# Performance work log

Hardware: AMD Instinct MI355X
Metric: run time of the kernel (lower is better)

The kernel has to match this reference:

```python
import jax, jax.numpy as jnp
import numpy as np

N_NODES = 100000
N_EDGES = 6400000


def setup_inputs() -> dict:
    key = jax.random.key(0)
    k1, k2, k3, k4, k5, k6 = jax.random.split(key, 6)
    x = jax.random.normal(k1, (N_NODES, 10), dtype=jnp.float32)
    edge_index = jax.random.randint(k2, (2, N_EDGES), 0, N_NODES, dtype=jnp.int64)
    # GCNConv(10,16) and GCNConv(16,2) parameters (glorot-ish scale)
    W1 = jax.random.normal(k3, (10, 16), dtype=jnp.float32) * (1.0 / np.sqrt(10))
    b1 = jnp.zeros((16,), dtype=jnp.float32)
    W2 = jax.random.normal(k4, (16, 2), dtype=jnp.float32) * (1.0 / np.sqrt(16))
    b2 = jnp.zeros((2,), dtype=jnp.float32)
    return {"x": x, "edge_index": edge_index, "W1": W1, "b1": b1, "W2": W2, "b2": b2}


def _gcn_conv(h, src, dst, norm, W, b, n_nodes):
    # PyG GCNConv: linear first, then normalized scatter-add aggregation
    h = h @ W                                   # [N, out]
    msg = h[src] * norm[:, None]                # gather + per-edge scale
    out = jax.ops.segment_sum(msg, dst, num_segments=n_nodes)
    return out + b


def reference(x, edge_index, W1, b1, W2, b2):
    n_nodes = x.shape[0]
    loop = jnp.arange(n_nodes, dtype=edge_index.dtype)
    src = jnp.concatenate([edge_index[0], loop])  # self-loops added (PyG default)
    dst = jnp.concatenate([edge_index[1], loop])
    # symmetric normalization deg^{-1/2} A_hat deg^{-1/2} (deg from target index)
    deg = jax.ops.segment_sum(jnp.ones_like(dst, dtype=x.dtype), dst, num_segments=n_nodes)
    dinv = jnp.where(deg > 0, jax.lax.rsqrt(deg), 0.0)
    norm = dinv[src] * dinv[dst]                 # [E+N]
    h = _gcn_conv(x, src, dst, norm, W1, b1, n_nodes)
    h = jax.nn.relu(h)
    out = _gcn_conv(h, src, dst, norm, W2, b2, n_nodes)
    return out
```

## Files before the change

### kernel.cpp

```cpp
#include <hip/hip_runtime.h>
#include <hip/hip_fp16.h>


#define BKT_BITS  8
#define BKT_SZ    256
#define NBK       512
#define NBLKA     256
#define TPB_A     1024
#define TPB_B     512
#define DST_SHIFT 24
#define SRC_MASK  0xFFFFFFu
#define XS_BYTES  32

static __device__ __forceinline__ int nt_src(const void* ei, int is64, int n_edges, unsigned e) {
    return is64 ? (int)__builtin_nontemporal_load(&((const long long*)ei)[e])
                : __builtin_nontemporal_load(&((const int*)ei)[e]);
}
static __device__ __forceinline__ int nt_dst(const void* ei, int is64, int n_edges, unsigned e) {
    return is64 ? (int)__builtin_nontemporal_load(&((const long long*)ei)[(unsigned)n_edges + e])
                : __builtin_nontemporal_load(&((const int*)ei)[(unsigned)n_edges + e]);
}

static __device__ __forceinline__ float2 h2f(unsigned w) {
    __half2 h = *(__half2*)&w;
    return __half22float2(h);
}

static __global__ void detect64_kernel(const unsigned int* __restrict__ w, int* flag) {
    __shared__ int nz;
    if (threadIdx.x == 0) nz = 0;
    __syncthreads();
    int local = 0;
    for (int k = threadIdx.x; k < 4096; k += blockDim.x)
        if (w[2 * k + 1] != 0u) local = 1;
    if (local) atomicOr(&nz, 1);
    __syncthreads();
    if (threadIdx.x == 0) *flag = (nz == 0) ? 1 : 0;
}

static __global__ void histA_kernel(const void* __restrict__ ei, const int* __restrict__ flag,
                                    unsigned* __restrict__ histA, int n_edges) {
    __shared__ unsigned h[NBK];
    for (int i = threadIdx.x; i < NBK; i += TPB_A) h[i] = 0u;
    __syncthreads();
    const int is64 = *flag;
    unsigned stride = gridDim.x * blockDim.x;
    for (unsigned e = blockIdx.x * blockDim.x + threadIdx.x; e < (unsigned)n_edges; e += stride) {
        int d = nt_dst(ei, is64, n_edges, e);
        atomicAdd(&h[(unsigned)d >> BKT_BITS], 1u);
    }
    __syncthreads();
    for (int i = threadIdx.x; i < NBK; i += TPB_A)
        histA[blockIdx.x * NBK + i] = h[i];
}

static __global__ void scan1_kernel(unsigned* __restrict__ histA, unsigned* __restrict__ total) {
    __shared__ unsigned s0[NBLKA], s1[NBLKA];
    const int b = blockIdx.x;
    const int t = threadIdx.x;
    unsigned v = histA[t * NBK + b];
    unsigned* a = s0; unsigned* c = s1;
    a[t] = v;
    __syncthreads();
    for (int off = 1; off < NBLKA; off <<= 1) {
        c[t] = a[t] + (t >= off ? a[t - off] : 0u);
        __syncthreads();
        unsigned* tmp = a; a = c; c = tmp;
    }
    histA[t * NBK + b] = a[t] - v;
    if (t == NBLKA - 1) total[b] = a[NBLKA - 1];
}

static __global__ void scan2_kernel(const unsigned* __restrict__ total,
                                    unsigned* __restrict__ bucket_base) {
    __shared__ unsigned s0[NBK], s1[NBK];
    const int t = threadIdx.x;
    unsigned v = total[t];
    unsigned* a = s0; unsigned* c = s1;
    a[t] = v;
    __syncthreads();
    for (int off = 1; off < NBK; off <<= 1) {
        c[t] = a[t] + (t >= off ? a[t - off] : 0u);
        __syncthreads();
        unsigned* tmp = a; a = c; c = tmp;
    }
    bucket_base[t] = a[t] - v;
}

static __global__ void scatterA_kernel(const void* __restrict__ ei, const int* __restrict__ flag,
                                       const unsigned* __restrict__ histA,
                                       const unsigned* __restrict__ bucket_base,
                                       unsigned* __restrict__ bucketed, int n_edges) {
    __shared__ unsigned cur[NBK];
    for (int i = threadIdx.x; i < NBK; i += TPB_A)
        cur[i] = bucket_base[i] + histA[blockIdx.x * NBK + i];
    __syncthreads();
    const int is64 = *flag;
    unsigned stride = gridDim.x * blockDim.x;
    for (unsigned e = blockIdx.x * blockDim.x + threadIdx.x; e < (unsigned)n_edges; e += stride) {
        unsigned s = (unsigned)nt_src(ei, is64, n_edges, e);
        unsigned d = (unsigned)nt_dst(ei, is64, n_edges, e);
        unsigned pos = atomicAdd(&cur[d >> BKT_BITS], 1u);
        bucketed[pos] = s | ((d & (BKT_SZ - 1u)) << DST_SHIFT);
    }
}

static __global__ void passB_kernel(const unsigned* __restrict__ bucketed,
                                    const unsigned* __restrict__ total,
                                    const unsigned* __restrict__ bucket_base,
                                    const float* __restrict__ x,
                                    unsigned* __restrict__ csr_src,
                                    unsigned* __restrict__ row_start,
                                    unsigned* __restrict__ cnt,
                                    float* __restrict__ dinv,
                                    char* __restrict__ xs, int n_nodes) {
    const int b = blockIdx.x;
    const int n0 = b << BKT_BITS;
    const int t = threadIdx.x;
    const unsigned base = bucket_base[b];
    const unsigned count = total[b];

    __shared__ unsigned h[BKT_SZ];
    __shared__ unsigned s0[BKT_SZ], s1[BKT_SZ];
    __shared__ unsigned cur[BKT_SZ];
    if (t < BKT_SZ) h[t] = 0u;
    __syncthreads();
    for (unsigned k = t; k < count; k += TPB_B)
        atomicAdd(&h[bucketed[base + k] >> DST_SHIFT], 1u);
    __syncthreads();
    unsigned* a = s0; unsigned* c = s1;
    if (t < BKT_SZ) a[t] = h[t];
    __syncthreads();
    for (int off = 1; off < BKT_SZ; off <<= 1) {
        if (t < BKT_SZ) c[t] = a[t] + (t >= off ? a[t - off] : 0u);
        __syncthreads();
        unsigned* tmp = a; a = c; c = tmp;
    }
    if (t < BKT_SZ) {
        unsigned excl = a[t] - h[t];
        cur[t] = excl;
        int n = n0 + t;
        if (n < n_nodes) {
            row_start[n] = base + excl;
            cnt[n] = h[t];
            float di = rsqrtf((float)(h[t] + 1u));
            dinv[n] = di;
            unsigned w[5];
#pragma unroll
            for (int j = 0; j < 5; j++) {
                unsigned lo = __half_as_ushort(__float2half_rn(x[(size_t)n * 10 + 2 * j] * di));
                unsigned hi = __half_as_ushort(__float2half_rn(x[(size_t)n * 10 + 2 * j + 1] * di));
                w[j] = lo | (hi << 16);
            }
            char* row = xs + (size_t)n * XS_BYTES;
            *(uint4*)row = make_uint4(w[0], w[1], w[2], w[3]);
            *(uint2*)(row + 16) = make_uint2(w[4], 0u);
        }
    }
    __syncthreads();
    for (unsigned k = t; k < count; k += TPB_B) {
        unsigned w = bucketed[base + k];
        unsigned pos = base + atomicAdd(&cur[w >> DST_SHIFT], 1u);
        csr_src[pos] = w & SRC_MASK;
    }
}

static __global__ void node1_kernel(const float* __restrict__ x, const float* __restrict__ dinv,
                                    char* __restrict__ xs, int n_nodes) {
    int i = blockIdx.x * blockDim.x + threadIdx.x;
    if (i >= n_nodes) return;
    float di = dinv[i];
    unsigned w[5];
#pragma unroll
    for (int j = 0; j < 5; j++) {
        unsigned lo = __half_as_ushort(__float2half_rn(x[(size_t)i * 10 + 2 * j] * di));
        unsigned hi = __half_as_ushort(__float2half_rn(x[(size_t)i * 10 + 2 * j + 1] * di));
        w[j] = lo | (hi << 16);
    }
    char* row = xs + (size_t)i * XS_BYTES;
    *(uint4*)row = make_uint4(w[0], w[1], w[2], w[3]);
    *(uint2*)(row + 16) = make_uint2(w[4], 0u);
}

static __global__ void gather1_kernel(const unsigned int* __restrict__ row_start,
                                      const unsigned int* __restrict__ cnt,
                                      const unsigned int* __restrict__ csr_src,
                                      const char* __restrict__ xs,
                                      const float* __restrict__ dinv,
                                      const float* __restrict__ W1, const float* __restrict__ b1,
                                      const float* __restrict__ W2,
                                      float* __restrict__ gs, int n_nodes) {
    __shared__ float sW1[160];
    __shared__ float sb1[16];
    __shared__ float sW2[32];
    for (int k = threadIdx.x; k < 160; k += blockDim.x) sW1[k] = W1[k];
    if (threadIdx.x < 16) sb1[threadIdx.x] = b1[threadIdx.x];
    if (threadIdx.x < 32) sW2[threadIdx.x] = W2[threadIdx.x];
    __syncthreads();
    int node = blockIdx.x * (blockDim.x >> 4) + (threadIdx.x >> 4);
    int lg = threadIdx.x & 15;
    if (node >= n_nodes) return;
    unsigned start = row_start[node];
    unsigned degn = cnt[node];
    float acc[10];
#pragma unroll
    for (int j = 0; j < 10; j++) acc[j] = 0.f;
    for (unsigned k = lg; k < degn; k += 16) {
        unsigned s = __builtin_nontemporal_load(&csr_src[start + k]);
        const char* row = xs + (size_t)s * XS_BYTES;
        uint4 a = *(const uint4*)row;
        unsigned b = *(const unsigned*)(row + 16);
        float2 f;
        f = h2f(a.x); acc[0] += f.x; acc[1] += f.y;
        f = h2f(a.y); acc[2] += f.x; acc[3] += f.y;
        f = h2f(a.z); acc[4] += f.x; acc[5] += f.y;
        f = h2f(a.w); acc[6] += f.x; acc[7] += f.y;
        f = h2f(b);   acc[8] += f.x; acc[9] += f.y;
    }
    if (lg == 0) {
        const char* row = xs + (size_t)node * XS_BYTES;
        uint4 a = *(const uint4*)row;
        unsigned b = *(const unsigned*)(row + 16);
        float2 f;
        f = h2f(a.x); acc[0] += f.x; acc[1] += f.y;
        f = h2f(a.y); acc[2] += f.x; acc[3] += f.y;
        f = h2f(a.z); acc[4] += f.x; acc[5] += f.y;
        f = h2f(a.w); acc[6] += f.x; acc[7] += f.y;
        f = h2f(b);   acc[8] += f.x; acc[9] += f.y;
    }
#pragma unroll
    for (int off = 8; off > 0; off >>= 1) {
#pragma unroll
        for (int j = 0; j < 10; j++) acc[j] += __shfl_xor(acc[j], off);
    }
    float di = dinv[node];
    float h = sb1[lg];
#pragma unroll
    for (int k = 0; k < 10; k++) h = fmaf(acc[k] * di, sW1[k * 16 + lg], h);
    h = fmaxf(h, 0.f);
    float g0 = h * sW2[lg * 2 + 0];
    float g1 = h * sW2[lg * 2 + 1];
#pragma unroll
    for (int off = 8; off > 0; off >>= 1) {
        g0 += __shfl_xor(g0, off);
        g1 += __shfl_xor(g1, off);
    }
    if (lg == 0) {
        float2 o;
        o.x = g0 * di;
        o.y = g1 * di;
        ((float2*)gs)[node] = o;
    }
}

static __global__ void gather2_kernel(const unsigned int* __restrict__ row_start,
                                      const unsigned int* __restrict__ cnt,
                                      const unsigned int* __restrict__ csr_src,
                                      const float* __restrict__ gs,
                                      const float* __restrict__ dinv,
                                      const float* __restrict__ b2,
                                      float* __restrict__ out, int n_nodes) {
    int node = blockIdx.x * (blockDim.x >> 4) + (threadIdx.x >> 4);
    int lg = threadIdx.x & 15;
    if (node >= n_nodes) return;
    unsigned start = row_start[node];
    unsigned degn = cnt[node];
    float a0 = 0.f, a1 = 0.f;
    const float2* G = (const float2*)gs;
    for (unsigned k = lg; k < degn; k += 16) {
        unsigned s = __builtin_nontemporal_load(&csr_src[start + k]);
        float2 v = G[s];
        a0 += v.x; a1 += v.y;
    }
    if (lg == 0) {
        float2 s = G[node];
        a0 += s.x; a1 += s.y;
    }
#pragma unroll
    for (int off = 8; off > 0; off >>= 1) {
        a0 += __shfl_xor(a0, off);
        a1 += __shfl_xor(a1, off);
    }
    if (lg == 0) {
        float di = dinv[node];
        float2 o;
        o.x = fmaf(a0, di, b2[0]);
        o.y = fmaf(a1, di, b2[1]);
        ((float2*)out)[node] = o;
    }
}

static __global__ void deg_kernel(const void* __restrict__ ei, const int* __restrict__ flag,
                                  unsigned int* __restrict__ cnt, int n_edges) {
    const int is64 = *flag;
    unsigned stride = gridDim.x * blockDim.x;
    for (unsigned e = blockIdx.x * blockDim.x + threadIdx.x; e < (unsigned)n_edges; e += stride) {
        int d = nt_dst(ei, is64, n_edges, e);
        atomicAdd(&cnt[d], 1u);
    }
}
static __global__ void alloc_kernel(const unsigned int* __restrict__ cnt,
                                    unsigned int* __restrict__ row_start,
                                    unsigned int* __restrict__ cursor,
                                    unsigned int* __restrict__ gcur,
                                    float* __restrict__ dinv, int n_nodes) {
    __shared__ unsigned wsum[4];
    int i = blockIdx.x * blockDim.x + threadIdx.x;
    int lane = threadIdx.x & 63;
    int wid = threadIdx.x >> 6;
    unsigned d = (i < n_nodes) ? cnt[i] : 0u;
    unsigned scan = d;
#pragma unroll
    for (int off = 1; off < 64; off <<= 1) {
        unsigned t = __shfl_up(scan, off);
        if (lane >= off) scan += t;
    }
    if (lane == 63) wsum[wid] = scan;
    __syncthreads();
    if (threadIdx.x == 0) {
        unsigned s0 = wsum[0], s1 = wsum[1], s2 = wsum[2], s3 = wsum[3];
        unsigned base = atomicAdd(gcur, s0 + s1 + s2 + s3);
        wsum[0] = base;
        wsum[1] = base + s0;
        wsum[2] = base + s0 + s1;
        wsum[3] = base + s0 + s1 + s2;
    }
    __syncthreads();
    if (i < n_nodes) {
        unsigned pos = wsum[wid] + scan - d;
        row_start[i] = pos;
        cursor[i] = pos;
        dinv[i] = rsqrtf((float)(d + 1u));
    }
}
static __global__ void csrfill_kernel(const void* __restrict__ ei, const int* __restrict__ flag,
                                      unsigned int* __restrict__ cursor,
                                      unsigned int* __restrict__ csr_src, int n_edges) {
    const int is64 = *flag;
    unsigned stride = gridDim.x * blockDim.x;
    for (unsigned e = blockIdx.x * blockDim.x + threadIdx.x; e < (unsigned)n_edges; e += stride) {
        int s = nt_src(ei, is64, n_edges, e);
        int d = nt_dst(ei, is64, n_edges, e);
        unsigned pos = atomicAdd(&cursor[d], 1u);
        csr_src[pos] = (unsigned)s;
    }
}

static inline char* align_up(char* p, size_t a) {
    return (char*)(((uintptr_t)p + a - 1) & ~(uintptr_t)(a - 1));
}

extern "C" void kernel_launch(void* const* d_in, const int* in_sizes, int n_in,
                              void* d_out, int out_size, void* d_ws, size_t ws_size,
                              hipStream_t stream) {
    const float* x  = (const float*)d_in[0];
    const void*  ei = d_in[1];
    const float* W1 = (const float*)d_in[2];
    const float* b1 = (const float*)d_in[3];
    const float* W2 = (const float*)d_in[4];
    const float* b2 = (const float*)d_in[5];
    float* out = (float*)d_out;

    const int n_nodes = in_sizes[0] / 10;
    const int n_edges = in_sizes[1] / 2;
    (void)n_in; (void)out_size;

    const int nbuckets = (n_nodes + BKT_SZ - 1) >> BKT_BITS;
    const bool pack_ok = (n_nodes <= (1 << DST_SHIFT)) && (nbuckets <= NBK);

    char* p = (char*)d_ws;
    int* flag = (int*)p;
    unsigned* gcur = (unsigned*)(p + 64);
    p += 256;
    unsigned* row_start = (unsigned*)p; p = align_up(p + (size_t)n_nodes * 4, 256);
    unsigned* cnt = (unsigned*)p;       p = align_up(p + (size_t)n_nodes * 4, 256);
    float* dinv = (float*)p;            p = align_up(p + (size_t)n_nodes * 4, 256);
    float* gs = (float*)p;              p = align_up(p + (size_t)n_nodes * 8, 256);
    char* xs = p;                       p = align_up(p + (size_t)n_nodes * XS_BYTES, 256);
    unsigned* csr_src = (unsigned*)p;   p = align_up(p + (size_t)n_edges * 4, 256);

    const size_t base_bytes = (size_t)(p - (char*)d_ws);
    const size_t need_new = base_bytes + (size_t)NBLKA * NBK * 4 + 2 * (size_t)NBK * 4 + 1024 +
                            (size_t)n_edges * 4;
    const size_t need_old = base_bytes + (size_t)n_nodes * 4 + 256;

    const int NODES_PER_BLK = 256 / 16;
    const int gblocks = (n_nodes + NODES_PER_BLK - 1) / NODES_PER_BLK;

    if (pack_ok && ws_size >= need_new) {
        unsigned* histA = (unsigned*)p;       p = align_up(p + (size_t)NBLKA * NBK * 4, 256);
        unsigned* total = (unsigned*)p;       p = align_up(p + (size_t)NBK * 4, 256);
        unsigned* bucket_base = (unsigned*)p; p = align_up(p + (size_t)NBK * 4, 256);
        unsigned* bucketed = (unsigned*)p;    p = align_up(p + (size_t)n_edges * 4, 256);

        detect64_kernel<<<1, 256, 0, stream>>>((const unsigned int*)ei, flag);
        histA_kernel<<<NBLKA, TPB_A, 0, stream>>>(ei, flag, histA, n_edges);
        scan1_kernel<<<NBK, NBLKA, 0, stream>>>(histA, total);
        scan2_kernel<<<1, NBK, 0, stream>>>(total, bucket_base);
        scatterA_kernel<<<NBLKA, TPB_A, 0, stream>>>(ei, flag, histA, bucket_base, bucketed, n_edges);
        passB_kernel<<<nbuckets, TPB_B, 0, stream>>>(bucketed, total, bucket_base, x, csr_src,
                                                     row_start, cnt, dinv, xs, n_nodes);
        gather1_kernel<<<gblocks, 256, 0, stream>>>(row_start, cnt, csr_src, xs, dinv,
                                                    W1, b1, W2, gs, n_nodes);
        gather2_kernel<<<gblocks, 256, 0, stream>>>(row_start, cnt, csr_src, gs, dinv,
                                                    b2, out, n_nodes);
    } else if (ws_size >= need_old) {
        unsigned* cursor = (unsigned*)p;

        hipMemsetAsync(d_ws, 0, 256, stream);
        hipMemsetAsync(cnt, 0, (size_t)n_nodes * 4, stream);
        detect64_kernel<<<1, 256, 0, stream>>>((const unsigned int*)ei, flag);
        deg_kernel<<<2048, 256, 0, stream>>>(ei, flag, cnt, n_edges);
        alloc_kernel<<<(n_nodes + 255) / 256, 256, 0, stream>>>(cnt, row_start, cursor, gcur, dinv, n_nodes);
        csrfill_kernel<<<4096, 256, 0, stream>>>(ei, flag, cursor, csr_src, n_edges);
        node1_kernel<<<(n_nodes + 255) / 256, 256, 0, stream>>>(x, dinv, xs, n_nodes);
        gather1_kernel<<<gblocks, 256, 0, stream>>>(row_start, cnt, csr_src, xs, dinv,
                                                    W1, b1, W2, gs, n_nodes);
        gather2_kernel<<<gblocks, 256, 0, stream>>>(row_start, cnt, csr_src, gs, dinv,
                                                    b2, out, n_nodes);
    }
}
```

Baseline: 243.2 us.

## Vectorize edge loads, enlarge grids, replicate passB histograms, drop nontemporal CSR loads

The histogram and scatter passes now have each thread read two adjacent edge indices with one wide load, falling back to scalar loads when the edge count is odd. The pass-A grid and the pass-B block size are doubled. Pass B spreads its per-bucket counting atomics over four shared-memory histogram copies to cut atomic contention. The gather kernels load csr_src with ordinary loads instead of nontemporal ones. Together these aim to cut memory-instruction count and LDS atomic conflicts, at the cost of more shared memory per block and larger blocks that may lower occupancy.

Result: faster. 227.3 us (-6.6%).

```diff
diff --git a/kernel.cpp b/kernel.cpp
--- a/kernel.cpp
+++ b/kernel.cpp
@@ -5,9 +5,9 @@
 #define BKT_BITS  8
 #define BKT_SZ    256
 #define NBK       512
-#define NBLKA     256
+#define NBLKA     512
 #define TPB_A     1024
-#define TPB_B     512
+#define TPB_B     1024
 #define DST_SHIFT 24
 #define SRC_MASK  0xFFFFFFu
 #define XS_BYTES  32
@@ -19,6 +19,22 @@
 static __device__ __forceinline__ int nt_dst(const void* ei, int is64, int n_edges, unsigned e) {
     return is64 ? (int)__builtin_nontemporal_load(&((const long long*)ei)[(unsigned)n_edges + e])
                 : __builtin_nontemporal_load(&((const int*)ei)[(unsigned)n_edges + e]);
+}
+static __device__ __forceinline__ void load_pair(const void* ei, int is64, int n_edges,
+                                                 unsigned e, int half,
+                                                 unsigned& v0, unsigned& v1) {
+    if (is64) {
+        const unsigned long long* p =
+            (const unsigned long long*)ei + (size_t)half * n_edges + e;
+        unsigned long long a = __builtin_nontemporal_load(p);
+        unsigned long long b = __builtin_nontemporal_load(p + 1);
+        v0 = (unsigned)a; v1 = (unsigned)b;
+    } else {
+        const unsigned long long* p =
+            (const unsigned long long*)((const int*)ei + (size_t)half * n_edges + e);
+        unsigned long long a = __builtin_nontemporal_load(p);
+        v0 = (unsigned)a; v1 = (unsigned)(a >> 32);
+    }
 }
 
 static __device__ __forceinline__ float2 h2f(unsigned w) {
@@ -44,10 +60,21 @@
     for (int i = threadIdx.x; i < NBK; i += TPB_A) h[i] = 0u;
     __syncthreads();
     const int is64 = *flag;
-    unsigned stride = gridDim.x * blockDim.x;
-    for (unsigned e = blockIdx.x * blockDim.x + threadIdx.x; e < (unsigned)n_edges; e += stride) {
-        int d = nt_dst(ei, is64, n_edges, e);
-        atomicAdd(&h[(unsigned)d >> BKT_BITS], 1u);
+    unsigned gid = blockIdx.x * blockDim.x + threadIdx.x;
+    if ((n_edges & 1) == 0) {
+        unsigned stride2 = gridDim.x * blockDim.x * 2u;
+        for (unsigned e = gid * 2u; e < (unsigned)n_edges; e += stride2) {
+            unsigned d0, d1;
+            load_pair(ei, is64, n_edges, e, 1, d0, d1);
+            atomicAdd(&h[d0 >> BKT_BITS], 1u);
+            atomicAdd(&h[d1 >> BKT_BITS], 1u);
+        }
+    } else {
+        unsigned stride = gridDim.x * blockDim.x;
+        for (unsigned e = gid; e < (unsigned)n_edges; e += stride) {
+            int d = nt_dst(ei, is64, n_edges, e);
+            atomicAdd(&h[(unsigned)d >> BKT_BITS], 1u);
+        }
     }
     __syncthreads();
     for (int i = threadIdx.x; i < NBK; i += TPB_A)
@@ -96,12 +123,26 @@
         cur[i] = bucket_base[i] + histA[blockIdx.x * NBK + i];
     __syncthreads();
     const int is64 = *flag;
-    unsigned stride = gridDim.x * blockDim.x;
-    for (unsigned e = blockIdx.x * blockDim.x + threadIdx.x; e < (unsigned)n_edges; e += stride) {
-        unsigned s = (unsigned)nt_src(ei, is64, n_edges, e);
-        unsigned d = (unsigned)nt_dst(ei, is64, n_edges, e);
-        unsigned pos = atomicAdd(&cur[d >> BKT_BITS], 1u);
-        bucketed[pos] = s | ((d & (BKT_SZ - 1u)) << DST_SHIFT);
+    unsigned gid = blockIdx.x * blockDim.x + threadIdx.x;
+    if ((n_edges & 1) == 0) {
+        unsigned stride2 = gridDim.x * blockDim.x * 2u;
+        for (unsigned e = gid * 2u; e < (unsigned)n_edges; e += stride2) {
+            unsigned s0, s1, d0, d1;
+            load_pair(ei, is64, n_edges, e, 0, s0, s1);
+            load_pair(ei, is64, n_edges, e, 1, d0, d1);
+            unsigned p0 = atomicAdd(&cur[d0 >> BKT_BITS], 1u);
+            unsigned p1 = atomicAdd(&cur[d1 >> BKT_BITS], 1u);
+            bucketed[p0] = s0 | ((d0 & (BKT_SZ - 1u)) << DST_SHIFT);
+            bucketed[p1] = s1 | ((d1 & (BKT_SZ - 1u)) << DST_SHIFT);
+        }
+    } else {
+        unsigned stride = gridDim.x * blockDim.x;
+        for (unsigned e = gid; e < (unsigned)n_edges; e += stride) {
+            unsigned s = (unsigned)nt_src(ei, is64, n_edges, e);
+            unsigned d = (unsigned)nt_dst(ei, is64, n_edges, e);
+            unsigned pos = atomicAdd(&cur[d >> BKT_BITS], 1u);
+            bucketed[pos] = s | ((d & (BKT_SZ - 1u)) << DST_SHIFT);
+        }
     }
 }
 
@@ -120,16 +161,21 @@
     const unsigned base = bucket_base[b];
     const unsigned count = total[b];
 
-    __shared__ unsigned h[BKT_SZ];
+    __shared__ unsigned h4[4][BKT_SZ];
     __shared__ unsigned s0[BKT_SZ], s1[BKT_SZ];
     __shared__ unsigned cur[BKT_SZ];
-    if (t < BKT_SZ) h[t] = 0u;
-    __syncthreads();
+    for (int i = t; i < 4 * BKT_SZ; i += TPB_B) ((unsigned*)h4)[i] = 0u;
+    __syncthreads();
+    const int copy = (t >> 8) & 3;
     for (unsigned k = t; k < count; k += TPB_B)
-        atomicAdd(&h[bucketed[base + k] >> DST_SHIFT], 1u);
-    __syncthreads();
+        atomicAdd(&h4[copy][bucketed[base + k] >> DST_SHIFT], 1u);
+    __syncthreads();
+    unsigned hv = 0;
     unsigned* a = s0; unsigned* c = s1;
-    if (t < BKT_SZ) a[t] = h[t];
+    if (t < BKT_SZ) {
+        hv = h4[0][t] + h4[1][t] + h4[2][t] + h4[3][t];
+        a[t] = hv;
+    }
     __syncthreads();
     for (int off = 1; off < BKT_SZ; off <<= 1) {
         if (t < BKT_SZ) c[t] = a[t] + (t >= off ? a[t - off] : 0u);
@@ -137,13 +183,13 @@
         unsigned* tmp = a; a = c; c = tmp;
     }
     if (t < BKT_SZ) {
-        unsigned excl = a[t] - h[t];
+        unsigned excl = a[t] - hv;
         cur[t] = excl;
         int n = n0 + t;
         if (n < n_nodes) {
             row_start[n] = base + excl;
-            cnt[n] = h[t];
-            float di = rsqrtf((float)(h[t] + 1u));
+            cnt[n] = hv;
+            float di = rsqrtf((float)(hv + 1u));
             dinv[n] = di;
             unsigned w[5];
 #pragma unroll
@@ -206,7 +252,7 @@
 #pragma unroll
     for (int j = 0; j < 10; j++) acc[j] = 0.f;
     for (unsigned k = lg; k < degn; k += 16) {
-        unsigned s = __builtin_nontemporal_load(&csr_src[start + k]);
+        unsigned s = csr_src[start + k];
         const char* row = xs + (size_t)s * XS_BYTES;
         uint4 a = *(const uint4*)row;
         unsigned b = *(const unsigned*)(row + 16);
@@ -268,8 +314,7 @@
     float a0 = 0.f, a1 = 0.f;
     const float2* G = (const float2*)gs;
     for (unsigned k = lg; k < degn; k += 16) {
-        unsigned s = __builtin_nontemporal_load(&csr_src[start + k]);
-        float2 v = G[s];
+        float2 v = G[csr_src[start + k]];
         a0 += v.x; a1 += v.y;
     }
     if (lg == 0) {
```
